# Kernel tuning notes

Measured on AMD Instinct MI355X. Metric: run time of the kernel, lower is better.

## Reference

```python
import jax, jax.numpy as jnp
import numpy as np

B, N, D = 1, 4096, 320
HEADS, DIM_HEAD = 8, 40
PHASE, Hm, Wm = 3, 64, 64  # guidance mask spatial dims; Hm*Wm == N


def setup_inputs() -> dict:
    key = jax.random.key(0)
    ks = jax.random.split(key, 7)
    s = 0.02
    x = jax.random.normal(ks[0], (B, N, D), jnp.float32)
    guidance_mask = jax.random.bernoulli(ks[1], 0.25, (B, PHASE, Hm, Wm)).astype(jnp.float32)
    Wq = jax.random.normal(ks[2], (D, HEADS * DIM_HEAD), jnp.float32) * s
    Wk = jax.random.normal(ks[3], (D, HEADS * DIM_HEAD), jnp.float32) * s
    Wv = jax.random.normal(ks[4], (D, HEADS * DIM_HEAD), jnp.float32) * s
    Wo = jax.random.normal(ks[5], (HEADS * DIM_HEAD, D), jnp.float32) * s
    bo = jnp.zeros((D,), jnp.float32)
    return {"x": x, "guidance_mask": guidance_mask, "Wq": Wq, "Wk": Wk,
            "Wv": Wv, "Wo": Wo, "bo": bo}


def reference(x, guidance_mask, Wq, Wk, Wv, Wo, bo):
    b, n, _ = x.shape
    h, dh = HEADS, DIM_HEAD
    scale = dh ** (-0.5)

    def split_heads(t):
        # b n (h d) -> (b h) n d
        return t.reshape(b, n, h, dh).transpose(0, 2, 1, 3).reshape(b * h, n, dh)

    q = split_heads(x @ Wq)
    k = split_heads(x @ Wk)
    v = split_heads(x @ Wv)

    sim = jnp.einsum('bid,bjd->bij', q, k) * scale  # (b*h, n, n)

    _, p, Hh, Ww = guidance_mask.shape
    HW = Hh * Ww  # == n
    g = guidance_mask.reshape(b, p, HW)
    # sum over phases of outer products, clamped at 1 (binary block mask)
    mask_sim = jnp.minimum(jnp.einsum('bpi,bpj->bij', g, g), 1.0)  # (b, HW, HW)
    mask_sim = jnp.repeat(mask_sim, h, axis=0)  # (b*h, HW, HW), heads within each b

    neg = -jnp.finfo(sim.dtype).max
    # original: sim[:, :, :HW][mask_sim == 0] = -max ; here n == HW so full matrix
    sim = jnp.where(mask_sim == 0, neg, sim)

    attn = jax.nn.softmax(sim, axis=-1)
    out = jnp.einsum('bij,bjd->bid', attn, v)  # (b*h, n, dh)
    out = out.reshape(b, h, n, dh).transpose(0, 2, 1, 3).reshape(b, n, h * dh)
    return out @ Wo + bo
```

## Files before the change

kernel.cpp:

```cpp
#include <hip/hip_runtime.h>
#include <hip/hip_bf16.h>
#include <stdint.h>

#define NT 4096
#define DM 320
#define NH 8
#define DH 40
#define KS 4
#define QSCALE 0.22811013f
#define PSTR 68
#define KFJB 640

typedef float f32x4 __attribute__((ext_vector_type(4)));
typedef __bf16 bf16x8 __attribute__((ext_vector_type(8)));

__device__ __forceinline__ unsigned short f2b(float f) {
  unsigned u = __builtin_bit_cast(unsigned, f);
  u += 0x7FFFu + ((u >> 16) & 1u);
  return (unsigned short)(u >> 16);
}

__device__ __forceinline__ bf16x8 ld_bf8(const unsigned short* p) {
  uint4 v = *(const uint4*)p;
  return __builtin_bit_cast(bf16x8, v);
}

__device__ __forceinline__ f32x4 mfma16(bf16x8 a, bf16x8 b, f32x4 c) {
  return __builtin_amdgcn_mfma_f32_16x16x32_bf16(a, b, c, 0, 0, 0);
}

__device__ __forceinline__ float fexp2(float x) {
#if __has_builtin(__builtin_amdgcn_exp2f)
  return __builtin_amdgcn_exp2f(x);
#else
  float r; asm("v_exp_f32 %0, %1" : "=v"(r) : "v"(x)); return r;
#endif
}

__device__ __forceinline__ uint2 pack4(float a, float b, float c, float d) {
  uint2 pk;
  pk.x = (unsigned)f2b(a) | ((unsigned)f2b(b) << 16);
  pk.y = (unsigned)f2b(c) | ((unsigned)f2b(d) << 16);
  return pk;
}

__device__ __forceinline__ uint4 idfrag(int idx) {
  uint4 r;
  r.x = (idx == 0 ? 0x3F80u : 0u) | (idx == 1 ? 0x3F800000u : 0u);
  r.y = (idx == 2 ? 0x3F80u : 0u) | (idx == 3 ? 0x3F800000u : 0u);
  r.z = (idx == 4 ? 0x3F80u : 0u) | (idx == 5 ? 0x3F800000u : 0u);
  r.w = (idx == 6 ? 0x3F80u : 0u) | (idx == 7 ? 0x3F800000u : 0u);
  return r;
}

__device__ __forceinline__ size_t fmi(int tile, int nk, int k, int o) {
  return ((size_t)tile * nk + (k >> 5)) * 512 + (size_t)((k >> 3) & 3) * 128 +
         (size_t)(o & 15) * 8 + (k & 7);
}

__global__ __launch_bounds__(256) void prep_kernel(
    const float* __restrict__ x, const float* __restrict__ g,
    const float* __restrict__ Wq, const float* __restrict__ Wk,
    const float* __restrict__ Wv, const float* __restrict__ Wo,
    unsigned short* __restrict__ xbf, unsigned char* __restrict__ sgp,
    unsigned short* __restrict__ Wtf, int* __restrict__ perm,
    int* __restrict__ invp, int* __restrict__ nqp) {
  const int b = blockIdx.x, t = threadIdx.x;
  if (b == 100) {
    __shared__ int cnt[256];
    unsigned char mys[16];
    int c1 = 0;
#pragma unroll
    for (int i = 0; i < 16; ++i) {
      int tok = t * 16 + i;
      unsigned s = 0;
      if (g[tok] != 0.f)          s |= 1u;
      if (g[NT + tok] != 0.f)     s |= 2u;
      if (g[2 * NT + tok] != 0.f) s |= 4u;
      mys[i] = (unsigned char)s;
      c1 += (s != 0u);
    }
    cnt[t] = c1;
    __syncthreads();
    for (int off = 1; off < 256; off <<= 1) {
      int v = (t >= off) ? cnt[t - off] : 0;
      __syncthreads();
      cnt[t] += v;
      __syncthreads();
    }
    const int nq = cnt[255];
    int p1 = cnt[t] - c1;
    int p0 = nq + (t * 16 - p1);
#pragma unroll
    for (int i = 0; i < 16; ++i) {
      int tok = t * 16 + i;
      if (mys[i] != 0) { perm[p1] = tok; invp[tok] = p1; sgp[p1] = mys[i]; p1++; }
      else             { perm[p0] = tok; invp[tok] = p0; sgp[p0] = 0;      p0++; }
    }
    if (t == 0) nqp[0] = nq;
    return;
  }
  if (b > 100) {
    int base = (b - 101) * 2560;
#pragma unroll
    for (int j = 0; j < 10; ++j) {
      int i = (base + j * 256 + t) * 4;
      int m = i / DM, k = i % DM;
      float4 v = *(const float4*)(x + i);
      ushort4 u;
      u.x = f2b(v.x); u.y = f2b(v.y); u.z = f2b(v.z); u.w = f2b(v.w);
      *(ushort4*)(xbf + fmi(m >> 4, 10, k, m)) = u;
    }
    return;
  }
  __shared__ __align__(16) unsigned short lt[64 * 72];
  int kx = b % 5, cy = b / 5;
  int cm = cy % 5;
  const float* src;
  int rowbase;
  if (cy < 5)       { src = Wq; rowbase = cm * 64; }
  else if (cy < 10) { src = Wk; rowbase = 320 + cm * 64; }
  else if (cy < 15) { src = Wv; rowbase = 640 + cm * 64; }
  else              { src = Wo; rowbase = 960 + cm * 64; }
  const int c0 = cm * 64;
  const int k0 = kx * 64;
#pragma unroll
  for (int i = 0; i < 4; ++i) {
    int kr = (t >> 4) + i * 16, cc = (t & 15) * 4;
    float4 w4 = *(const float4*)&src[(size_t)(k0 + kr) * DM + c0 + cc];
    lt[(cc + 0) * 72 + kr] = f2b(w4.x);
    lt[(cc + 1) * 72 + kr] = f2b(w4.y);
    lt[(cc + 2) * 72 + kr] = f2b(w4.z);
    lt[(cc + 3) * 72 + kr] = f2b(w4.w);
  }
  __syncthreads();
#pragma unroll
  for (int i = 0; i < 2; ++i) {
    int idx = t + i * 256, cl = idx >> 3, ch = idx & 7;
    int c = rowbase + cl, k = k0 + ch * 8;
    *(uint4*)&Wtf[fmi(c >> 4, 10, k, c)] = *(const uint4*)&lt[cl * 72 + ch * 8];
  }
}

__global__ __launch_bounds__(256, 4) void qkv_gemm(
    const unsigned short* __restrict__ xbf, const unsigned short* __restrict__ Wtf,
    const int* __restrict__ invp,
    unsigned short* __restrict__ Qb, unsigned short* __restrict__ Kf,
    unsigned short* __restrict__ Vk) {
  const int t = threadIdx.x;
  const int w = t >> 6, lane = t & 63, quad = lane >> 4, ln = lane & 15;
  const int m0 = blockIdx.x * 64;
  const int cy = blockIdx.y;
  const int a = cy / 5;
  const int cc0 = (cy % 5) * 64;
  const int mt = (m0 >> 4) + w;
  const int ct0 = a * 20 + (cc0 >> 4);

  f32x4 acc[4] = {{0,0,0,0},{0,0,0,0},{0,0,0,0},{0,0,0,0}};
  for (int kc = 0; kc < 10; ++kc) {
    bf16x8 xf = ld_bf8(xbf + ((size_t)(mt * 10 + kc)) * 512 + lane * 8);
#pragma unroll
    for (int nt = 0; nt < 4; ++nt) {
      bf16x8 wf = ld_bf8(Wtf + ((size_t)((ct0 + nt) * 10 + kc)) * 512 + lane * 8);
      acc[nt] = mfma16(wf, xf, acc[nt]);
    }
  }
  const int bp = invp[m0 + w * 16 + ln];
  if (a == 0) {
#pragma unroll
    for (int nt = 0; nt < 4; ++nt) {
      int c = cc0 + nt * 16 + quad * 4;
      int h = c / DH, d = c % DH;
      uint2 pk = pack4(acc[nt][0] * QSCALE, acc[nt][1] * QSCALE,
                       acc[nt][2] * QSCALE, acc[nt][3] * QSCALE);
      *(uint2*)&Qb[((size_t)h * NT + bp) * 64 + d] = pk;
    }
  } else {
    unsigned short* dst = (a == 1) ? Kf : Vk;
#pragma unroll
    for (int nt = 0; nt < 4; ++nt) {
      int c = cc0 + nt * 16 + quad * 4;
      int h = c / DH, d = c % DH;
      uint2 pk = pack4(acc[nt][0], acc[nt][1], acc[nt][2], acc[nt][3]);
      size_t base = ((size_t)h * 256 + (bp >> 4)) * KFJB;
      size_t idx = (d < 32)
          ? base + (size_t)(d >> 3) * 128 + (size_t)(bp & 15) * 8 + (d & 7)
          : base + 512 + (size_t)(bp & 15) * 8 + (d - 32);
      *(uint2*)&dst[idx] = pk;
    }
  }
}

__global__ __launch_bounds__(256) void retile_kernel(
    const unsigned short* __restrict__ Vk, unsigned short* __restrict__ Vf) {
  const int t = threadIdx.x;
  const int w = t >> 6, lane = t & 63, ln = lane & 15, jg = lane >> 4;
  const bf16x8 b1f = __builtin_bit_cast(bf16x8, idfrag(ln - jg * 8));
  const bf16x8 b2f = __builtin_bit_cast(bf16x8, idfrag(ln + 16 - jg * 8));
  const uint4 z4 = {0, 0, 0, 0};
#pragma unroll
  for (int i = 0; i < 4; ++i) {
    const int task = (blockIdx.x * 4 + w) * 4 + i;
    const int h = task >> 8, jb = task & 255;
    const unsigned short* kb = Vk + ((size_t)h * 256 + jb) * KFJB;
    uint4 f0 = *(const uint4*)(kb + lane * 8);
    uint4 f1 = z4;
    if (lane < 16) f1 = *(const uint4*)(kb + 512 + lane * 8);
    f32x4 d1 = {0,0,0,0}, d2 = {0,0,0,0}, d3 = {0,0,0,0};
    d1 = mfma16(__builtin_bit_cast(bf16x8, f0), b1f, d1);
    d2 = mfma16(__builtin_bit_cast(bf16x8, f0), b2f, d2);
    d3 = mfma16(__builtin_bit_cast(bf16x8, f1), b1f, d3);
    const int bp = jb * 16 + jg * 4;
#pragma unroll
    for (int ot = 0; ot < 3; ++ot) {
      int dd = ot * 16 + ln;
      if (ot == 2 && ln >= 8) continue;
      f32x4 dv = (ot == 0) ? d1 : (ot == 1) ? d2 : d3;
      size_t idx = ((((((size_t)(h * 64 + (bp >> 6)) * 3 + (dd >> 4)) * 2 +
                       ((bp >> 5) & 1)) * 4 + ((bp >> 3) & 3)) * 16 + (dd & 15))) * 8 +
                   (bp & 7);
      *(uint2*)&Vf[idx] = pack4(dv[0], dv[1], dv[2], dv[3]);
    }
  }
}

__global__ __launch_bounds__(256, 4) void attn_kernel(
    const unsigned short* __restrict__ Qb, const unsigned short* __restrict__ Kf,
    const unsigned short* __restrict__ Vf, const unsigned char* __restrict__ sgp,
    const int* __restrict__ nqp,
    unsigned short* __restrict__ Opf, float* __restrict__ Lpart,
    unsigned short* __restrict__ Ubf) {
  __shared__ __align__(16) unsigned short pt[4][32 * PSTR];
  __shared__ float vs[4][48];
  const int t = threadIdx.x;
  const int w = t >> 6, lane = t & 63, quad = lane >> 4, ln = lane & 15;
  const int h = blockIdx.y, sp = blockIdx.z;
  const int nq = nqp[0];
  const int nkt = (nq + 63) >> 6;
  const int nq_pad = (nq + 127) & ~127;

  const unsigned short* Vfh = Vf + (size_t)h * 196608;
  const uint4 z4 = {0, 0, 0, 0};
  const uint4 ones4 = {0x3F803F80u, 0x3F803F80u, 0x3F803F80u, 0x3F803F80u};
  const bf16x8 onesb = __builtin_bit_cast(bf16x8, ones4);

  if (blockIdx.x == 32) {
    if (sp != 0) return;
    f32x4 o[3] = {{0,0,0,0},{0,0,0,0},{0,0,0,0}};
    for (int jt = w; jt < 64; jt += 4) {
#pragma unroll
      for (int ot = 0; ot < 3; ++ot) {
        uint4 v0 = *(const uint4*)(Vfh + ((size_t)((jt * 3 + ot) * 2 + 0)) * 512 +
                                   lane * 8);
        uint4 v1 = *(const uint4*)(Vfh + ((size_t)((jt * 3 + ot) * 2 + 1)) * 512 +
                                   lane * 8);
        o[ot] = mfma16(__builtin_bit_cast(bf16x8, v0), onesb, o[ot]);
        o[ot] = mfma16(__builtin_bit_cast(bf16x8, v1), onesb, o[ot]);
      }
    }
    if (ln == 0) {
#pragma unroll
      for (int ot = 0; ot < 3; ++ot)
#pragma unroll
        for (int r = 0; r < 4; ++r) vs[w][ot * 16 + quad * 4 + r] = o[ot][r];
    }
    __syncthreads();
    if (t < DH) {
      float s = vs[0][t] + vs[1][t] + vs[2][t] + vs[3][t];
      Ubf[h * DH + t] = f2b(s * (1.0f / (float)NT));
    }
    return;
  }

  const int qt = (blockIdx.x + 8 * sp) & 31;
  if (qt * 128 >= nq_pad) return;
  const int qrow = qt * 128 + w * 32;

  const unsigned short* Kfh = Kf + (size_t)h * 256 * KFJB;
  unsigned short* ptw = pt[w];
  const bool vone = (ln == 8);

  bf16x8 qa[2][2];
  unsigned sqx4[2];
  f32x4 o[3][2] = {{{0,0,0,0},{0,0,0,0}},{{0,0,0,0},{0,0,0,0}},{{0,0,0,0},{0,0,0,0}}};

#pragma unroll
  for (int tq = 0; tq < 2; ++tq) {
    int bp = qrow + tq * 16 + ln;
    const unsigned short* Qp = Qb + ((size_t)h * NT + bp) * 64;
    qa[tq][0] = ld_bf8(Qp + quad * 8);
    uint4 q1 = z4;
    if (quad == 0) q1 = *(const uint4*)(Qp + 32);
    qa[tq][1] = __builtin_bit_cast(bf16x8, q1);
    sqx4[tq] = (unsigned)sgp[bp] * 0x01010101u;
  }

  for (int jt = sp; jt < nkt; jt += KS) {
    uint4 kfr0[4], kfr1[4];
#pragma unroll
    for (int nt = 0; nt < 4; ++nt) {
      const unsigned short* kb = Kfh + (size_t)(jt * 4 + nt) * KFJB;
      kfr0[nt] = *(const uint4*)(kb + lane * 8);
      kfr1[nt] = z4;
      if (lane < 16) kfr1[nt] = *(const uint4*)(kb + 512 + lane * 8);
    }
#pragma unroll
    for (int nt = 0; nt < 4; ++nt) {
      bf16x8 ka0 = __builtin_bit_cast(bf16x8, kfr0[nt]);
      bf16x8 ka1 = __builtin_bit_cast(bf16x8, kfr1[nt]);
      unsigned spj = *(const unsigned*)(sgp + jt * 64 + nt * 16 + quad * 4);
#pragma unroll
      for (int tq = 0; tq < 2; ++tq) {
        f32x4 acc = {0.f, 0.f, 0.f, 0.f};
        acc = mfma16(ka0, qa[tq][0], acc);
        acc = mfma16(ka1, qa[tq][1], acc);
        unsigned m4 = spj & sqx4[tq];
        unsigned u[4];
#pragma unroll
        for (int r = 0; r < 4; ++r) {
          unsigned mb = (m4 >> (8 * r)) & 255u;
          float am = mb ? acc[r] : -3.0e38f;
          u[r] = __builtin_bit_cast(unsigned, fexp2(am));
        }
        uint2 pk;
        pk.x = (u[0] >> 16) | (u[1] & 0xffff0000u);
        pk.y = (u[2] >> 16) | (u[3] & 0xffff0000u);
        *(uint2*)&ptw[(tq * 16 + ln) * PSTR + nt * 16 + quad * 4] = pk;
      }
    }
    uint4 vfr[6];
#pragma unroll
    for (int ot = 0; ot < 3; ++ot)
#pragma unroll
      for (int c = 0; c < 2; ++c)
        vfr[ot * 2 + c] =
            *(const uint4*)(Vfh + ((size_t)((jt * 3 + ot) * 2 + c)) * 512 + lane * 8);
    if (vone) { vfr[4] = ones4; vfr[5] = ones4; }

    bf16x8 pb[2][2];
    asm volatile("s_waitcnt lgkmcnt(0)" ::: "memory");
#pragma unroll
    for (int tq = 0; tq < 2; ++tq) {
      pb[tq][0] = ld_bf8(&ptw[(tq * 16 + ln) * PSTR + quad * 8]);
      pb[tq][1] = ld_bf8(&ptw[(tq * 16 + ln) * PSTR + 32 + quad * 8]);
    }
#pragma unroll
    for (int ot = 0; ot < 3; ++ot) {
      bf16x8 va0 = __builtin_bit_cast(bf16x8, vfr[ot * 2]);
      bf16x8 va1 = __builtin_bit_cast(bf16x8, vfr[ot * 2 + 1]);
#pragma unroll
      for (int tq = 0; tq < 2; ++tq) {
        o[ot][tq] = mfma16(va0, pb[tq][0], o[ot][tq]);
        o[ot][tq] = mfma16(va1, pb[tq][1], o[ot][tq]);
      }
    }
  }

#pragma unroll
  for (int tq = 0; tq < 2; ++tq) {
    int bp = qrow + tq * 16 + ln;
#pragma unroll
    for (int ot = 0; ot < 3; ++ot) {
      int d0 = ot * 16 + quad * 4;
      if (d0 < DH) {
        int c = h * DH + d0;
        uint2 pk = pack4(o[ot][tq][0], o[ot][tq][1], o[ot][tq][2], o[ot][tq][3]);
        *(uint2*)&Opf[fmi(sp * 256 + (bp >> 4), 10, c, bp)] = pk;
      }
    }
    if (quad == 2)
      Lpart[sp * NT + bp] = o[2][tq][0];
  }
}

__global__ __launch_bounds__(256, 4) void combine_kernel(
    const unsigned short* __restrict__ Opf, const float* __restrict__ Lpart,
    const int* __restrict__ perm, const int* __restrict__ nqp,
    unsigned short* __restrict__ Abf) {
  const int t = threadIdx.x;
  const int w = t >> 6, lane = t & 63;
  const int task = blockIdx.x * 4 + w;
  const int tile = task / 10, kc = task % 10;
  const int nq_pad = (nqp[0] + 127) & ~127;
  if (tile * 16 >= nq_pad) return;
  const int row = tile * 16 + (lane & 15);

  float L = 0.f;
#pragma unroll
  for (int sp = 0; sp < KS; ++sp) L += Lpart[sp * NT + row];
  const float inv = 1.f / L;

  float s8[8] = {0, 0, 0, 0, 0, 0, 0, 0};
#pragma unroll
  for (int sp = 0; sp < KS; ++sp) {
    uint4 v = *(const uint4*)(Opf + ((size_t)((sp * 256 + tile) * 10 + kc)) * 512 +
                              lane * 8);
    unsigned vv[4] = {v.x, v.y, v.z, v.w};
#pragma unroll
    for (int j = 0; j < 4; ++j) {
      s8[2 * j]     += __builtin_bit_cast(float, vv[j] << 16);
      s8[2 * j + 1] += __builtin_bit_cast(float, vv[j] & 0xffff0000u);
    }
  }
  uint4 av;
  av.x = (unsigned)f2b(s8[0] * inv) | ((unsigned)f2b(s8[1] * inv) << 16);
  av.y = (unsigned)f2b(s8[2] * inv) | ((unsigned)f2b(s8[3] * inv) << 16);
  av.z = (unsigned)f2b(s8[4] * inv) | ((unsigned)f2b(s8[5] * inv) << 16);
  av.w = (unsigned)f2b(s8[6] * inv) | ((unsigned)f2b(s8[7] * inv) << 16);
  const int m = perm[row];
  *(uint4*)&Abf[fmi(m >> 4, 10, kc * 32 + (lane >> 4) * 8, m)] = av;
}

__global__ __launch_bounds__(256, 4) void out_gemm(
    const unsigned short* __restrict__ Abf, const unsigned short* __restrict__ Wtf,
    const float* __restrict__ bo, const int* __restrict__ invp,
    const int* __restrict__ nqp, const unsigned short* __restrict__ Ubf,
    float* __restrict__ out) {
  const int t = threadIdx.x;
  const int w = t >> 6, lane = t & 63, quad = lane >> 4, ln = lane & 15;
  const int m0 = blockIdx.x * 64;
  const int cc0 = blockIdx.y * 64;
  const int mt = (m0 >> 4) + w;
  const int m = m0 + w * 16 + ln;
  const int ct0 = 60 + (cc0 >> 4);
  const bool uni = invp[m] >= nqp[0];

  f32x4 acc[4] = {{0,0,0,0},{0,0,0,0},{0,0,0,0},{0,0,0,0}};
  for (int kc = 0; kc < 10; ++kc) {
    uint4 uv = *(const uint4*)(Ubf + kc * 32 + quad * 8);
    uint4 av = *(const uint4*)(Abf + ((size_t)(mt * 10 + kc)) * 512 + lane * 8);
    if (uni) av = uv;
    bf16x8 af = __builtin_bit_cast(bf16x8, av);
#pragma unroll
    for (int nt = 0; nt < 4; ++nt) {
      bf16x8 wf = ld_bf8(Wtf + ((size_t)((ct0 + nt) * 10 + kc)) * 512 + lane * 8);
      acc[nt] = mfma16(wf, af, acc[nt]);
    }
  }
#pragma unroll
  for (int nt = 0; nt < 4; ++nt) {
    int c = cc0 + nt * 16 + quad * 4;
    float4 bv = *(const float4*)(bo + c);
    float4 ov;
    ov.x = acc[nt][0] + bv.x;
    ov.y = acc[nt][1] + bv.y;
    ov.z = acc[nt][2] + bv.z;
    ov.w = acc[nt][3] + bv.w;
    *(float4*)(out + (size_t)m * DM + c) = ov;
  }
}

extern "C" void kernel_launch(void* const* d_in, const int* in_sizes, int n_in,
                              void* d_out, int out_size, void* d_ws, size_t ws_size,
                              hipStream_t stream) {
  const float* x  = (const float*)d_in[0];
  const float* g  = (const float*)d_in[1];
  const float* Wq = (const float*)d_in[2];
  const float* Wk = (const float*)d_in[3];
  const float* Wv = (const float*)d_in[4];
  const float* Wo = (const float*)d_in[5];
  const float* bo = (const float*)d_in[6];
  float* out = (float*)d_out;

  char* ws = (char*)d_ws;
  const size_t SGP_OFF  = 0;
  const size_t NQ_OFF   = 4096;
  const size_t PERM_OFF = 8192;
  const size_t INV_OFF  = 24576;
  const size_t XBF_OFF  = 40960;
  const size_t WTF_OFF = XBF_OFF + (size_t)NT * DM * 2;
  const size_t QB_OFF  = WTF_OFF + (size_t)1280 * DM * 2;
  const size_t KF_OFF  = QB_OFF + (size_t)NH * NT * 64 * 2;
  const size_t VK_OFF  = KF_OFF + (size_t)NH * 256 * KFJB * 2;
  const size_t VF_OFF  = VK_OFF + (size_t)NH * 256 * KFJB * 2;
  const size_t OPF_OFF = VF_OFF + (size_t)NH * 196608 * 2;
  const size_t LP_OFF  = OPF_OFF + (size_t)KS * 256 * 10 * 512 * 2;
  const size_t UBF_OFF = LP_OFF + (size_t)KS * NT * 4;
  const size_t ABF_OFF = UBF_OFF + 4096;
  unsigned char* sgp   = (unsigned char*)(ws + SGP_OFF);
  int* nqp             = (int*)(ws + NQ_OFF);
  int* perm            = (int*)(ws + PERM_OFF);
  int* invp            = (int*)(ws + INV_OFF);
  unsigned short* xbf  = (unsigned short*)(ws + XBF_OFF);
  unsigned short* Wtf  = (unsigned short*)(ws + WTF_OFF);
  unsigned short* Qb   = (unsigned short*)(ws + QB_OFF);
  unsigned short* Kf   = (unsigned short*)(ws + KF_OFF);
  unsigned short* Vk   = (unsigned short*)(ws + VK_OFF);
  unsigned short* Vf   = (unsigned short*)(ws + VF_OFF);
  unsigned short* Opf  = (unsigned short*)(ws + OPF_OFF);
  float* Lpart         = (float*)(ws + LP_OFF);
  unsigned short* Ubf  = (unsigned short*)(ws + UBF_OFF);
  unsigned short* Abf  = (unsigned short*)(ws + ABF_OFF);

  prep_kernel<<<229, 256, 0, stream>>>(x, g, Wq, Wk, Wv, Wo, xbf, sgp, Wtf,
                                       perm, invp, nqp);
  qkv_gemm<<<dim3(64, 15), 256, 0, stream>>>(xbf, Wtf, invp, Qb, Kf, Vk);
  retile_kernel<<<128, 256, 0, stream>>>(Vk, Vf);
  attn_kernel<<<dim3(33, NH, KS), 256, 0, stream>>>(Qb, Kf, Vf, sgp, nqp,
                                                    Opf, Lpart, Ubf);
  combine_kernel<<<640, 256, 0, stream>>>(Opf, Lpart, perm, nqp, Abf);
  out_gemm<<<dim3(64, 5), 256, 0, stream>>>(Abf, Wtf, bo, invp, nqp, Ubf, out);
}
```

Baseline: 130.9 us.

## Sort tokens by phase signature and skip fully masked key tiles

```diff
diff --git a/kernel.cpp b/kernel.cpp
--- a/kernel.cpp
+++ b/kernel.cpp
@@ -64,12 +64,13 @@
     const float* __restrict__ Wv, const float* __restrict__ Wo,
     unsigned short* __restrict__ xbf, unsigned char* __restrict__ sgp,
     unsigned short* __restrict__ Wtf, int* __restrict__ perm,
-    int* __restrict__ invp, int* __restrict__ nqp) {
+    int* __restrict__ invp, int* __restrict__ nqp,
+    unsigned char* __restrict__ tsig) {
   const int b = blockIdx.x, t = threadIdx.x;
   if (b == 100) {
-    __shared__ int cnt[256];
+    __shared__ unsigned long long sa[256], sb[256];
     unsigned char mys[16];
-    int c1 = 0;
+    unsigned long long ca = 0ull, cb = 0ull;
 #pragma unroll
     for (int i = 0; i < 16; ++i) {
       int tok = t * 16 + i;
@@ -78,26 +79,58 @@
       if (g[NT + tok] != 0.f)     s |= 2u;
       if (g[2 * NT + tok] != 0.f) s |= 4u;
       mys[i] = (unsigned char)s;
-      c1 += (s != 0u);
-    }
-    cnt[t] = c1;
+      if (s < 4) ca += 1ull << (16 * s);
+      else       cb += 1ull << (16 * (s - 4));
+    }
+    sa[t] = ca; sb[t] = cb;
     __syncthreads();
     for (int off = 1; off < 256; off <<= 1) {
-      int v = (t >= off) ? cnt[t - off] : 0;
+      unsigned long long va = (t >= off) ? sa[t - off] : 0ull;
+      unsigned long long vb = (t >= off) ? sb[t - off] : 0ull;
       __syncthreads();
-      cnt[t] += v;
+      sa[t] += va; sb[t] += vb;
       __syncthreads();
     }
-    const int nq = cnt[255];
-    int p1 = cnt[t] - c1;
-    int p0 = nq + (t * 16 - p1);
+    const unsigned long long ta = sa[255], tb = sb[255];
+    const int t1 = (int)((ta >> 16) & 0xffff), t2 = (int)((ta >> 32) & 0xffff),
+              t3 = (int)((ta >> 48) & 0xffff), t4 = (int)(tb & 0xffff),
+              t5 = (int)((tb >> 16) & 0xffff), t6 = (int)((tb >> 32) & 0xffff),
+              t7 = (int)((tb >> 48) & 0xffff);
+    const int b1 = 0, b2 = t1, b3 = b2 + t2, b4 = b3 + t3, b5 = b4 + t4,
+              b6 = b5 + t5, b7 = b6 + t6, b0 = b7 + t7;
+    unsigned long long ra = sa[t] - ca;
+    unsigned long long rb = sb[t] - cb;
+    ra += ((unsigned long long)(unsigned)b0)        |
+          ((unsigned long long)(unsigned)b1 << 16)  |
+          ((unsigned long long)(unsigned)b2 << 32)  |
+          ((unsigned long long)(unsigned)b3 << 48);
+    rb += ((unsigned long long)(unsigned)b4)        |
+          ((unsigned long long)(unsigned)b5 << 16)  |
+          ((unsigned long long)(unsigned)b6 << 32)  |
+          ((unsigned long long)(unsigned)b7 << 48);
 #pragma unroll
     for (int i = 0; i < 16; ++i) {
       int tok = t * 16 + i;
-      if (mys[i] != 0) { perm[p1] = tok; invp[tok] = p1; sgp[p1] = mys[i]; p1++; }
-      else             { perm[p0] = tok; invp[tok] = p0; sgp[p0] = 0;      p0++; }
-    }
-    if (t == 0) nqp[0] = nq;
+      unsigned s = mys[i];
+      int sh = 16 * (int)(s & 3u);
+      int p;
+      if (s < 4) { p = (int)((ra >> sh) & 0xffff); ra += 1ull << sh; }
+      else       { p = (int)((rb >> sh) & 0xffff); rb += 1ull << sh; }
+      perm[p] = tok; invp[tok] = p; sgp[p] = (unsigned char)s;
+    }
+    if (t == 0) nqp[0] = b0;
+    if (t < 64) {
+      const int lo = t * 64, hi = lo + 64;
+      unsigned o = 0;
+      if (b1 < hi && b2 > lo && b2 > b1) o |= 1u;
+      if (b2 < hi && b3 > lo && b3 > b2) o |= 2u;
+      if (b3 < hi && b4 > lo && b4 > b3) o |= 3u;
+      if (b4 < hi && b5 > lo && b5 > b4) o |= 4u;
+      if (b5 < hi && b6 > lo && b6 > b5) o |= 5u;
+      if (b6 < hi && b7 > lo && b7 > b6) o |= 6u;
+      if (b7 < hi && b0 > lo && b0 > b7) o |= 7u;
+      tsig[t] = (unsigned char)o;
+    }
     return;
   }
   if (b > 100) {
@@ -227,7 +260,7 @@
 __global__ __launch_bounds__(256, 4) void attn_kernel(
     const unsigned short* __restrict__ Qb, const unsigned short* __restrict__ Kf,
     const unsigned short* __restrict__ Vf, const unsigned char* __restrict__ sgp,
-    const int* __restrict__ nqp,
+    const int* __restrict__ nqp, const unsigned char* __restrict__ tsg,
     unsigned short* __restrict__ Opf, float* __restrict__ Lpart,
     unsigned short* __restrict__ Ubf) {
   __shared__ __align__(16) unsigned short pt[4][32 * PSTR];
@@ -276,6 +309,13 @@
   if (qt * 128 >= nq_pad) return;
   const int qrow = qt * 128 + w * 32;
 
+  unsigned qv = *(const unsigned*)(sgp + qrow)      | *(const unsigned*)(sgp + qrow + 4)
+              | *(const unsigned*)(sgp + qrow + 8)  | *(const unsigned*)(sgp + qrow + 12)
+              | *(const unsigned*)(sgp + qrow + 16) | *(const unsigned*)(sgp + qrow + 20)
+              | *(const unsigned*)(sgp + qrow + 24) | *(const unsigned*)(sgp + qrow + 28);
+  qv |= qv >> 16; qv |= qv >> 8;
+  const unsigned qor = qv & 255u;
+
   const unsigned short* Kfh = Kf + (size_t)h * 256 * KFJB;
   unsigned short* ptw = pt[w];
   const bool vone = (ln == 8);
@@ -296,6 +336,7 @@
   }
 
   for (int jt = sp; jt < nkt; jt += KS) {
+    if ((tsg[jt] & qor) == 0) continue;
     uint4 kfr0[4], kfr1[4];
 #pragma unroll
     for (int nt = 0; nt < 4; ++nt) {
@@ -465,6 +506,7 @@
   char* ws = (char*)d_ws;
   const size_t SGP_OFF  = 0;
   const size_t NQ_OFF   = 4096;
+  const size_t TSIG_OFF = 4224;
   const size_t PERM_OFF = 8192;
   const size_t INV_OFF  = 24576;
   const size_t XBF_OFF  = 40960;
@@ -479,6 +521,7 @@
   const size_t ABF_OFF = UBF_OFF + 4096;
   unsigned char* sgp   = (unsigned char*)(ws + SGP_OFF);
   int* nqp             = (int*)(ws + NQ_OFF);
+  unsigned char* tsig  = (unsigned char*)(ws + TSIG_OFF);
   int* perm            = (int*)(ws + PERM_OFF);
   int* invp            = (int*)(ws + INV_OFF);
   unsigned short* xbf  = (unsigned short*)(ws + XBF_OFF);
@@ -493,10 +536,10 @@
   unsigned short* Abf  = (unsigned short*)(ws + ABF_OFF);
 
   prep_kernel<<<229, 256, 0, stream>>>(x, g, Wq, Wk, Wv, Wo, xbf, sgp, Wtf,
-                                       perm, invp, nqp);
+                                       perm, invp, nqp, tsig);
   qkv_gemm<<<dim3(64, 15), 256, 0, stream>>>(xbf, Wtf, invp, Qb, Kf, Vk);
   retile_kernel<<<128, 256, 0, stream>>>(Vk, Vf);
-  attn_kernel<<<dim3(33, NH, KS), 256, 0, stream>>>(Qb, Kf, Vf, sgp, nqp,
+  attn_kernel<<<dim3(33, NH, KS), 256, 0, stream>>>(Qb, Kf, Vf, sgp, nqp, tsig,
                                                     Opf, Lpart, Ubf);
   combine_kernel<<<640, 256, 0, stream>>>(Opf, Lpart, perm, nqp, Abf);
   out_gemm<<<dim3(64, 5), 256, 0, stream>>>(Abf, Wtf, bo, invp, nqp, Ubf, out);
```

New measurement: 131.5 us. No clear change (+0.4%).
